# Kernel optimization log

Measured on AMD Instinct MI355X. Metric: run time of the kernel, lower is better.

## Reference

```python
import jax, jax.numpy as jnp
import numpy as np

N_NODES = 50000
N_EDGES = 800000
D_IN = 128
D_HID = 128
D_OUT = 128


def _gcn_layer(x, W, b, src, dst, norm):
    # dense projection then edge-weighted gather -> scatter-add at dst
    h = x @ W                                   # [N, d_out]
    msg = h[src] * norm[:, None]                # [E, d_out]
    out = jax.ops.segment_sum(msg, dst, num_segments=N_NODES)
    return out + b


def setup_inputs() -> dict:
    key = jax.random.key(0)
    k = jax.random.split(key, 8)
    x = jax.random.normal(k[0], (N_NODES, D_IN), dtype=jnp.float32)
    edge_index = jax.random.randint(k[1], (2, N_EDGES), 0, N_NODES, dtype=jnp.int64)
    edge_weight = jax.random.uniform(k[2], (N_EDGES,), dtype=jnp.float32)
    # GCNConv params (glorot-ish scale)
    s1 = 1.0 / np.sqrt(D_IN)
    s2 = 1.0 / np.sqrt(D_HID)
    W1 = jax.random.normal(k[3], (D_IN, D_HID), dtype=jnp.float32) * s1
    b1 = jnp.zeros((D_HID,), dtype=jnp.float32)
    W2 = jax.random.normal(k[4], (D_HID, D_OUT), dtype=jnp.float32) * s2
    b2 = jnp.zeros((D_OUT,), dtype=jnp.float32)
    return {"x": x, "edge_index": edge_index, "edge_weight": edge_weight,
            "W1": W1, "b1": b1, "W2": W2, "b2": b2}


def reference(x, edge_index, edge_weight, W1, b1, W2, b2):
    src, dst = edge_index[0], edge_index[1]
    # gcn_norm (add_self_loops=False): deg from scatter-add of edge_weight at dst
    deg = jax.ops.segment_sum(edge_weight, dst, num_segments=N_NODES)
    dinv = jnp.where(deg > 0, jax.lax.rsqrt(jnp.maximum(deg, 1e-30)), 0.0)
    norm = dinv[src] * edge_weight * dinv[dst]  # [E]
    h = jax.nn.relu(_gcn_layer(x, W1, b1, src, dst, norm))
    out = _gcn_layer(h, W2, b2, src, dst, norm)
    # F.dropout in eval mode (deterministic reference) is identity
    return out
```

## Files before the change

kernel.cpp:

```cpp
#include <hip/hip_runtime.h>

#define N_NODES 50000
#define N_EDGES 800000
#define D 128
#define MAXDEG 64
#define NBUCK 196
#define BUCKCAP 5120
#define EPB 4096
#define NBB 196

typedef __attribute__((ext_vector_type(8))) short bf16x8;
typedef __attribute__((ext_vector_type(4))) float f32x4;

__device__ inline unsigned short f2bf(float f) {
    unsigned u = __float_as_uint(f);
    unsigned r = (u + 0x7fffu + ((u >> 16) & 1u)) >> 16;
    return (unsigned short)r;
}

__global__ __launch_bounds__(256) void k_bucket(const int* __restrict__ src,
                                                const int* __restrict__ dst,
                                                const float* __restrict__ ew,
                                                int* __restrict__ cursor,
                                                uint2* __restrict__ buck,
                                                const float* __restrict__ W1,
                                                const float* __restrict__ W2,
                                                unsigned short* __restrict__ Wt1,
                                                unsigned short* __restrict__ Wt2) {
    if (blockIdx.x >= NBB) {
        const float* W = (blockIdx.x == NBB) ? W1 : W2;
        unsigned short* Wt = (blockIdx.x == NBB) ? Wt1 : Wt2;
        for (int idx = threadIdx.x; idx < D * D; idx += 256) {
            int n = idx & 127, k = idx >> 7;
            Wt[n * D + k] = f2bf(W[k * D + n]);
        }
        return;
    }
    __shared__ uint2 sorted[EPB];
    __shared__ int hist[NBUCK];
    __shared__ int scn[NBUCK];
    __shared__ int gbase[NBUCK];
    __shared__ int s[256];
    int tid = threadIdx.x;
    int e0 = blockIdx.x * EPB;
    for (int i = tid; i < NBUCK; i += 256) hist[i] = 0;
    __syncthreads();
    #pragma unroll
    for (int j = 0; j < 16; ++j) {
        int e = e0 + j * 256 + tid;
        if (e < N_EDGES) atomicAdd(&hist[dst[e] >> 8], 1);
    }
    __syncthreads();
    int v = tid < NBUCK ? hist[tid] : 0;
    s[tid] = v;
    __syncthreads();
    for (int off = 1; off < 256; off <<= 1) {
        int u = tid >= off ? s[tid - off] : 0;
        __syncthreads();
        s[tid] += u;
        __syncthreads();
    }
    int excl = s[tid] - v;
    if (tid < NBUCK) {
        scn[tid] = excl;
        gbase[tid] = v ? atomicAdd(&cursor[tid], v) : 0;
        hist[tid] = excl;
    }
    __syncthreads();
    #pragma unroll
    for (int j = 0; j < 16; ++j) {
        int e = e0 + j * 256 + tid;
        if (e < N_EDGES) {
            int d = dst[e];
            int sv = src[e];
            unsigned wf = min(__float2uint_rn(ew[e] * 65536.f), 65535u);
            int slot = atomicAdd(&hist[d >> 8], 1);
            sorted[slot] = make_uint2(((unsigned)sv << 16) | wf, (unsigned)d);
        }
    }
    __syncthreads();
    int total = min(EPB, N_EDGES - e0);
    for (int i = tid; i < total; i += 256) {
        uint2 en = sorted[i];
        int bk = (int)(en.y >> 8);
        int g = gbase[bk] + (i - scn[bk]);
        if (g < BUCKCAP)
            buck[(size_t)bk * BUCKCAP + g] = make_uint2(en.x, en.y & 255u);
    }
}

__global__ __launch_bounds__(256) void k_build(const int* __restrict__ cursor,
                                               const uint2* __restrict__ buck,
                                               unsigned* __restrict__ csr,
                                               int* __restrict__ cnt,
                                               float* __restrict__ dinv) {
    __shared__ unsigned csr_loc[256 * MAXDEG];
    __shared__ int cnt_loc[256];
    __shared__ int deg_loc[256];
    int b = blockIdx.x, tid = threadIdx.x;
    cnt_loc[tid] = 0;
    deg_loc[tid] = 0;
    __syncthreads();
    int n = min(cursor[b], BUCKCAP);
    const uint2* bb = buck + (size_t)b * BUCKCAP;
    for (int i = tid; i < n; i += 256) {
        uint2 e = bb[i];
        int ln = e.y;
        int slot = atomicAdd(&cnt_loc[ln], 1);
        if (slot < MAXDEG) csr_loc[ln * MAXDEG + slot] = e.x;
        atomicAdd(&deg_loc[ln], (int)(e.x & 0xffffu));
    }
    __syncthreads();
    int node0 = b * 256;
    int nnodes = min(256, N_NODES - node0);
    uint4* g = (uint4*)(csr + (size_t)node0 * MAXDEG);
    const uint4* l = (const uint4*)csr_loc;
    int nv = nnodes * (MAXDEG / 4);
    for (int i = tid; i < nv; i += 256) g[i] = l[i];
    if (tid < nnodes) {
        int node = node0 + tid;
        cnt[node] = min(cnt_loc[tid], MAXDEG);
        float sum = (float)deg_loc[tid] * (1.f / 65536.f);
        dinv[node] = sum > 0.f ? rsqrtf(fmaxf(sum, 1e-30f)) : 0.f;
    }
}

__global__ __launch_bounds__(256) void k_gemm(const float* __restrict__ X,
                                              const unsigned short* __restrict__ Wt,
                                              const float* __restrict__ dinv,
                                              unsigned short* __restrict__ Yb) {
    __shared__ unsigned short sX[64 * D];
    int row0 = blockIdx.x * 64;
    int nr = min(64, N_NODES - row0);
    {
        const float4* xs = (const float4*)(X + (size_t)row0 * D);
        int nvec = nr * (D / 4);
        for (int i = threadIdx.x; i < nvec; i += 256) {
            float4 v = xs[i];
            ushort4 o;
            o.x = f2bf(v.x); o.y = f2bf(v.y); o.z = f2bf(v.z); o.w = f2bf(v.w);
            *(ushort4*)(sX + i * 4) = o;
        }
    }
    __syncthreads();

    int wave = threadIdx.x >> 6, lane = threadIdx.x & 63;
    int m = lane & 15, quad = lane >> 4;
    f32x4 acc[8];
    #pragma unroll
    for (int i = 0; i < 8; ++i) acc[i] = (f32x4){0.f, 0.f, 0.f, 0.f};

    const unsigned short* aBase = sX + (wave * 16 + m) * D + quad * 8;
    #pragma unroll
    for (int c = 0; c < 4; ++c) {
        bf16x8 a = *(const bf16x8*)(aBase + c * 32);
        #pragma unroll
        for (int n0 = 0; n0 < 8; ++n0) {
            bf16x8 b = *(const bf16x8*)(Wt + (n0 * 16 + m) * D + c * 32 + quad * 8);
            acc[n0] = __builtin_amdgcn_mfma_f32_16x16x32_bf16(a, b, acc[n0], 0, 0, 0);
        }
    }

    float dv[4];
    #pragma unroll
    for (int i = 0; i < 4; ++i) {
        int r = row0 + wave * 16 + quad * 4 + i;
        dv[i] = r < N_NODES ? dinv[r] : 0.f;
    }

    unsigned short* sOut = sX + wave * 16 * D;
    __syncthreads();
    #pragma unroll
    for (int n0 = 0; n0 < 8; ++n0)
        #pragma unroll
        for (int i = 0; i < 4; ++i)
            sOut[(quad * 4 + i) * D + n0 * 16 + m] = f2bf(acc[n0][i] * dv[i]);
    __syncthreads();
    int rr = lane >> 2, c0 = (lane & 3) * 32;
    int grow = row0 + wave * 16 + rr;
    if (grow < N_NODES) {
        uint4* dstp = (uint4*)(Yb + (size_t)grow * D + c0);
        const uint4* srcp = (const uint4*)(sOut + rr * D + c0);
        dstp[0] = srcp[0]; dstp[1] = srcp[1]; dstp[2] = srcp[2]; dstp[3] = srcp[3];
    }
}

__global__ __launch_bounds__(256) void k_agg_mm(const unsigned short* __restrict__ H,
                                                const int* __restrict__ cnt,
                                                const unsigned* __restrict__ csr,
                                                const float* __restrict__ dinv,
                                                const float* __restrict__ b1,
                                                const unsigned short* __restrict__ Wt2,
                                                unsigned short* __restrict__ Hb) {
    __shared__ unsigned short sT[16 * D];
    int tid = threadIdx.x, wave = tid >> 6, lane = tid & 63;
    int g = lane >> 4, fl = lane & 15;
    int nb = blockIdx.x * 16;

    for (int nn = 0; nn < 4; ++nn) {
        int node = nb + wave * 4 + nn;
        int end = min(cnt[node], MAXDEG);
        int nw = (end + 15) >> 4;
        const uint4* row4 = (const uint4*)(csr + (size_t)node * MAXDEG);
        uint4 c4[4];
        #pragma unroll
        for (int w = 0; w < 4; ++w)
            if (w < nw) c4[w] = row4[w * 4 + g];
        float acc[8] = {0.f, 0.f, 0.f, 0.f, 0.f, 0.f, 0.f, 0.f};
        #pragma unroll
        for (int w = 0; w < 4; ++w) {
            if (w < nw) {
                int k0 = w * 16 + g * 4;
                unsigned cs[4] = {c4[w].x, c4[w].y, c4[w].z, c4[w].w};
                #pragma unroll
                for (int j = 0; j < 4; ++j) {
                    if (k0 + j < end) {
                        unsigned sv = cs[j] >> 16;
                        float nm = (float)(cs[j] & 0xffffu) * (1.f / 65536.f);
                        uint4 u = *(const uint4*)(H + (size_t)sv * D + fl * 8);
                        unsigned a0[4] = {u.x, u.y, u.z, u.w};
                        #pragma unroll
                        for (int q = 0; q < 4; ++q) {
                            acc[2 * q]     += __uint_as_float(a0[q] << 16) * nm;
                            acc[2 * q + 1] += __uint_as_float(a0[q] & 0xffff0000u) * nm;
                        }
                    }
                }
            }
        }
        #pragma unroll
        for (int j = 0; j < 8; ++j) {
            acc[j] += __shfl_xor(acc[j], 16, 64);
            acc[j] += __shfl_xor(acc[j], 32, 64);
        }
        if (g < 2) {
            float dn = dinv[node];
            int f = fl * 8 + g * 4;
            ushort4 o;
            o.x = f2bf(fmaxf(acc[g * 4 + 0] * dn + b1[f + 0], 0.f));
            o.y = f2bf(fmaxf(acc[g * 4 + 1] * dn + b1[f + 1], 0.f));
            o.z = f2bf(fmaxf(acc[g * 4 + 2] * dn + b1[f + 2], 0.f));
            o.w = f2bf(fmaxf(acc[g * 4 + 3] * dn + b1[f + 3], 0.f));
            *(ushort4*)(sT + (wave * 4 + nn) * D + f) = o;
        }
    }
    __syncthreads();

    int m = lane & 15, quad = lane >> 4;
    f32x4 acc2[2];
    acc2[0] = (f32x4){0.f, 0.f, 0.f, 0.f};
    acc2[1] = (f32x4){0.f, 0.f, 0.f, 0.f};
    #pragma unroll
    for (int c = 0; c < 4; ++c) {
        bf16x8 a = *(const bf16x8*)(sT + m * D + c * 32 + quad * 8);
        #pragma unroll
        for (int t = 0; t < 2; ++t) {
            int n0 = wave * 2 + t;
            bf16x8 b = *(const bf16x8*)(Wt2 + (n0 * 16 + m) * D + c * 32 + quad * 8);
            acc2[t] = __builtin_amdgcn_mfma_f32_16x16x32_bf16(a, b, acc2[t], 0, 0, 0);
        }
    }
    float dv[4];
    #pragma unroll
    for (int i = 0; i < 4; ++i) dv[i] = dinv[nb + quad * 4 + i];
    __syncthreads();
    #pragma unroll
    for (int t = 0; t < 2; ++t)
        #pragma unroll
        for (int i = 0; i < 4; ++i)
            sT[(quad * 4 + i) * D + (wave * 2 + t) * 16 + m] = f2bf(acc2[t][i] * dv[i]);
    __syncthreads();
    int rr = tid >> 4, cc = (tid & 15) * 8;
    *(uint4*)(Hb + (size_t)(nb + rr) * D + cc) = *(const uint4*)(sT + rr * D + cc);
}

__global__ __launch_bounds__(256) void k_aggregate(const unsigned short* __restrict__ H,
                                                   const int* __restrict__ cnt,
                                                   const unsigned* __restrict__ csr,
                                                   const float* __restrict__ dinv,
                                                   const float* __restrict__ bias,
                                                   float* __restrict__ out) {
    int node = blockIdx.x * 4 + (threadIdx.x >> 6);
    int lane = threadIdx.x & 63;
    int g = lane >> 4;
    int fl = lane & 15;
    int end = min(cnt[node], MAXDEG);
    int nw = (end + 15) >> 4;
    const uint4* row4 = (const uint4*)(csr + (size_t)node * MAXDEG);
    uint4 c4[4];
    #pragma unroll
    for (int w = 0; w < 4; ++w)
        if (w < nw) c4[w] = row4[w * 4 + g];
    float acc[8] = {0.f, 0.f, 0.f, 0.f, 0.f, 0.f, 0.f, 0.f};
    #pragma unroll
    for (int w = 0; w < 4; ++w) {
        if (w < nw) {
            int k0 = w * 16 + g * 4;
            unsigned cs[4] = {c4[w].x, c4[w].y, c4[w].z, c4[w].w};
            #pragma unroll
            for (int j = 0; j < 4; ++j) {
                if (k0 + j < end) {
                    unsigned sv = cs[j] >> 16;
                    float nm = (float)(cs[j] & 0xffffu) * (1.f / 65536.f);
                    uint4 u = *(const uint4*)(H + (size_t)sv * D + fl * 8);
                    unsigned a0[4] = {u.x, u.y, u.z, u.w};
                    #pragma unroll
                    for (int q = 0; q < 4; ++q) {
                        acc[2 * q]     += __uint_as_float(a0[q] << 16) * nm;
                        acc[2 * q + 1] += __uint_as_float(a0[q] & 0xffff0000u) * nm;
                    }
                }
            }
        }
    }
    #pragma unroll
    for (int j = 0; j < 8; ++j) {
        acc[j] += __shfl_xor(acc[j], 16, 64);
        acc[j] += __shfl_xor(acc[j], 32, 64);
    }
    if (g < 2) {
        float dn = dinv[node];
        int f = fl * 8 + g * 4;
        *(float4*)(out + (size_t)node * D + f) =
            make_float4(acc[g * 4 + 0] * dn + bias[f + 0],
                        acc[g * 4 + 1] * dn + bias[f + 1],
                        acc[g * 4 + 2] * dn + bias[f + 2],
                        acc[g * 4 + 3] * dn + bias[f + 3]);
    }
}

extern "C" void kernel_launch(void* const* d_in, const int* in_sizes, int n_in,
                              void* d_out, int out_size, void* d_ws, size_t ws_size,
                              hipStream_t stream) {
    const float* x   = (const float*)d_in[0];
    const int*   ei  = (const int*)d_in[1];
    const float* ew  = (const float*)d_in[2];
    const float* W1  = (const float*)d_in[3];
    const float* b1  = (const float*)d_in[4];
    const float* W2  = (const float*)d_in[5];
    const float* b2  = (const float*)d_in[6];
    float* out = (float*)d_out;

    const int* src = ei;
    const int* dst = ei + N_EDGES;

    char* base = (char*)d_ws;
    size_t off = 0;
    auto take = [&](size_t bytes) -> char* {
        char* p = base + off;
        off += (bytes + 255) & ~(size_t)255;
        return p;
    };
    int*      cursor = (int*)take(NBUCK * 4);
    size_t zero_bytes = off;
    float*    dinv = (float*)take(N_NODES * 4);
    int*      cnt  = (int*)take(N_NODES * 4);
    uint2*    buck = (uint2*)take((size_t)NBUCK * BUCKCAP * 8);
    unsigned* csr  = (unsigned*)take((size_t)N_NODES * MAXDEG * 4);
    unsigned short* Wt1 = (unsigned short*)take(D * D * 2);
    unsigned short* Wt2 = (unsigned short*)take(D * D * 2);
    unsigned short* h0  = (unsigned short*)take((size_t)N_NODES * D * 2);
    unsigned short* hb  = (unsigned short*)take((size_t)N_NODES * D * 2);

    hipMemsetAsync(d_ws, 0, zero_bytes, stream);

    const int GB = (N_NODES + 63) / 64;
    const int FB = N_NODES / 16;
    const int AB = N_NODES / 4;

    k_bucket<<<NBB + 2, 256, 0, stream>>>(src, dst, ew, cursor, buck,
                                          W1, W2, Wt1, Wt2);
    k_build<<<NBUCK, 256, 0, stream>>>(cursor, buck, csr, cnt, dinv);

    k_gemm<<<GB, 256, 0, stream>>>(x, Wt1, dinv, h0);
    k_agg_mm<<<FB, 256, 0, stream>>>(h0, cnt, csr, dinv, b1, Wt2, hb);
    k_aggregate<<<AB, 256, 0, stream>>>(hb, cnt, csr, dinv, b2, out);
}
```

Baseline: 214.1 us.

## Interleave two nodes' gathers per wave and pad shared tile rows

The fused aggregate+matmul kernel now processes its four nodes per wave as two interleaved pairs, issuing CSR and feature gathers for both nodes together. This gives each wave more independent loads in flight to hide gather latency. Shared-memory rows are also padded from 128 to 136 elements to reduce LDS bank conflicts in the MFMA operand reads and the transpose writes. The cost is higher register pressure, which may reduce occupancy.

After: 227.0 us. +6.0%, slower.

```diff
diff --git a/kernel.cpp b/kernel.cpp
--- a/kernel.cpp
+++ b/kernel.cpp
@@ -8,6 +8,7 @@
 #define BUCKCAP 5120
 #define EPB 4096
 #define NBB 196
+#define SP 136
 
 typedef __attribute__((ext_vector_type(8))) short bf16x8;
 typedef __attribute__((ext_vector_type(4))) float f32x4;
@@ -192,56 +193,88 @@
                                                 const float* __restrict__ b1,
                                                 const unsigned short* __restrict__ Wt2,
                                                 unsigned short* __restrict__ Hb) {
-    __shared__ unsigned short sT[16 * D];
+    __shared__ unsigned short sT[16 * SP];
     int tid = threadIdx.x, wave = tid >> 6, lane = tid & 63;
     int g = lane >> 4, fl = lane & 15;
     int nb = blockIdx.x * 16;
 
-    for (int nn = 0; nn < 4; ++nn) {
-        int node = nb + wave * 4 + nn;
-        int end = min(cnt[node], MAXDEG);
-        int nw = (end + 15) >> 4;
-        const uint4* row4 = (const uint4*)(csr + (size_t)node * MAXDEG);
-        uint4 c4[4];
-        #pragma unroll
-        for (int w = 0; w < 4; ++w)
-            if (w < nw) c4[w] = row4[w * 4 + g];
-        float acc[8] = {0.f, 0.f, 0.f, 0.f, 0.f, 0.f, 0.f, 0.f};
+    #pragma unroll
+    for (int p = 0; p < 2; ++p) {
+        int nodeA = nb + wave * 4 + 2 * p;
+        int nodeB = nodeA + 1;
+        int endA = min(cnt[nodeA], MAXDEG);
+        int endB = min(cnt[nodeB], MAXDEG);
+        int nwA = (endA + 15) >> 4;
+        int nwB = (endB + 15) >> 4;
+        const uint4* rowA = (const uint4*)(csr + (size_t)nodeA * MAXDEG);
+        const uint4* rowB = (const uint4*)(csr + (size_t)nodeB * MAXDEG);
+        uint4 cA[4], cB[4];
         #pragma unroll
         for (int w = 0; w < 4; ++w) {
-            if (w < nw) {
-                int k0 = w * 16 + g * 4;
-                unsigned cs[4] = {c4[w].x, c4[w].y, c4[w].z, c4[w].w};
+            if (w < nwA) cA[w] = rowA[w * 4 + g];
+            if (w < nwB) cB[w] = rowB[w * 4 + g];
+        }
+        float accA[8] = {0.f, 0.f, 0.f, 0.f, 0.f, 0.f, 0.f, 0.f};
+        float accB[8] = {0.f, 0.f, 0.f, 0.f, 0.f, 0.f, 0.f, 0.f};
+        #pragma unroll
+        for (int w = 0; w < 4; ++w) {
+            int k0 = w * 16 + g * 4;
+            if (w < nwA) {
+                unsigned cs[4] = {cA[w].x, cA[w].y, cA[w].z, cA[w].w};
                 #pragma unroll
                 for (int j = 0; j < 4; ++j) {
-                    if (k0 + j < end) {
+                    if (k0 + j < endA) {
                         unsigned sv = cs[j] >> 16;
                         float nm = (float)(cs[j] & 0xffffu) * (1.f / 65536.f);
                         uint4 u = *(const uint4*)(H + (size_t)sv * D + fl * 8);
                         unsigned a0[4] = {u.x, u.y, u.z, u.w};
                         #pragma unroll
                         for (int q = 0; q < 4; ++q) {
-                            acc[2 * q]     += __uint_as_float(a0[q] << 16) * nm;
-                            acc[2 * q + 1] += __uint_as_float(a0[q] & 0xffff0000u) * nm;
+                            accA[2 * q]     += __uint_as_float(a0[q] << 16) * nm;
+                            accA[2 * q + 1] += __uint_as_float(a0[q] & 0xffff0000u) * nm;
                         }
                     }
                 }
             }
+            if (w < nwB) {
+                unsigned cs[4] = {cB[w].x, cB[w].y, cB[w].z, cB[w].w};
+                #pragma unroll
+                for (int j = 0; j < 4; ++j) {
+                    if (k0 + j < endB) {
+                        unsigned sv = cs[j] >> 16;
+                        float nm = (float)(cs[j] & 0xffffu) * (1.f / 65536.f);
+                        uint4 u = *(const uint4*)(H + (size_t)sv * D + fl * 8);
+                        unsigned a0[4] = {u.x, u.y, u.z, u.w};
+                        #pragma unroll
+                        for (int q = 0; q < 4; ++q) {
+                            accB[2 * q]     += __uint_as_float(a0[q] << 16) * nm;
+                            accB[2 * q + 1] += __uint_as_float(a0[q] & 0xffff0000u) * nm;
+                        }
+                    }
+                }
+            }
         }
         #pragma unroll
         for (int j = 0; j < 8; ++j) {
-            acc[j] += __shfl_xor(acc[j], 16, 64);
-            acc[j] += __shfl_xor(acc[j], 32, 64);
+            accA[j] += __shfl_xor(accA[j], 16, 64);
+            accA[j] += __shfl_xor(accA[j], 32, 64);
+            accB[j] += __shfl_xor(accB[j], 16, 64);
+            accB[j] += __shfl_xor(accB[j], 32, 64);
         }
         if (g < 2) {
-            float dn = dinv[node];
             int f = fl * 8 + g * 4;
-            ushort4 o;
-            o.x = f2bf(fmaxf(acc[g * 4 + 0] * dn + b1[f + 0], 0.f));
-            o.y = f2bf(fmaxf(acc[g * 4 + 1] * dn + b1[f + 1], 0.f));
-            o.z = f2bf(fmaxf(acc[g * 4 + 2] * dn + b1[f + 2], 0.f));
-            o.w = f2bf(fmaxf(acc[g * 4 + 3] * dn + b1[f + 3], 0.f));
-            *(ushort4*)(sT + (wave * 4 + nn) * D + f) = o;
+            float dnA = dinv[nodeA], dnB = dinv[nodeB];
+            ushort4 oA, oB;
+            oA.x = f2bf(fmaxf(accA[g * 4 + 0] * dnA + b1[f + 0], 0.f));
+            oA.y = f2bf(fmaxf(accA[g * 4 + 1] * dnA + b1[f + 1], 0.f));
+            oA.z = f2bf(fmaxf(accA[g * 4 + 2] * dnA + b1[f + 2], 0.f));
+            oA.w = f2bf(fmaxf(accA[g * 4 + 3] * dnA + b1[f + 3], 0.f));
+            oB.x = f2bf(fmaxf(accB[g * 4 + 0] * dnB + b1[f + 0], 0.f));
+            oB.y = f2bf(fmaxf(accB[g * 4 + 1] * dnB + b1[f + 1], 0.f));
+            oB.z = f2bf(fmaxf(accB[g * 4 + 2] * dnB + b1[f + 2], 0.f));
+            oB.w = f2bf(fmaxf(accB[g * 4 + 3] * dnB + b1[f + 3], 0.f));
+            *(ushort4*)(sT + (wave * 4 + 2 * p) * SP + f) = oA;
+            *(ushort4*)(sT + (wave * 4 + 2 * p + 1) * SP + f) = oB;
         }
     }
     __syncthreads();
@@ -252,7 +285,7 @@
     acc2[1] = (f32x4){0.f, 0.f, 0.f, 0.f};
     #pragma unroll
     for (int c = 0; c < 4; ++c) {
-        bf16x8 a = *(const bf16x8*)(sT + m * D + c * 32 + quad * 8);
+        bf16x8 a = *(const bf16x8*)(sT + m * SP + c * 32 + quad * 8);
         #pragma unroll
         for (int t = 0; t < 2; ++t) {
             int n0 = wave * 2 + t;
@@ -268,10 +301,10 @@
     for (int t = 0; t < 2; ++t)
         #pragma unroll
         for (int i = 0; i < 4; ++i)
-            sT[(quad * 4 + i) * D + (wave * 2 + t) * 16 + m] = f2bf(acc2[t][i] * dv[i]);
+            sT[(quad * 4 + i) * SP + (wave * 2 + t) * 16 + m] = f2bf(acc2[t][i] * dv[i]);
     __syncthreads();
     int rr = tid >> 4, cc = (tid & 15) * 8;
-    *(uint4*)(Hb + (size_t)(nb + rr) * D + cc) = *(const uint4*)(sT + rr * D + cc);
+    *(uint4*)(Hb + (size_t)(nb + rr) * D + cc) = *(const uint4*)(sT + rr * SP + cc);
 }
 
 __global__ __launch_bounds__(256) void k_aggregate(const unsigned short* __restrict__ H,
```
